# Optimization experiments

Measured on AMD Instinct MI355X. Metric: run time of the kernel, lower is better.

## Reference

```python
import jax, jax.numpy as jnp
import numpy as np

L, B, S, D, F, H = 4, 2, 1024, 1024, 4096, 16
EPS = 1e-5


def setup_inputs() -> dict:
    key = jax.random.key(0)
    ks = jax.random.split(key, 15)
    w = lambda k, shape, s=0.02: (jax.random.normal(k, shape, jnp.float32) * s)
    inp = {
        "x": jax.random.normal(ks[0], (B, S, D), jnp.float32),
        # stacked per-layer params (scanned over leading L axis)
        "ln1_w": jnp.ones((L, D), jnp.float32),
        "ln1_b": jnp.zeros((L, D), jnp.float32),
        "Wq": w(ks[1], (L, D, D)),
        "Wk": w(ks[2], (L, D, D)),
        "Wv": w(ks[3], (L, D, D)),
        "Wo": w(ks[4], (L, D, D)),
        "bo": jnp.zeros((L, D), jnp.float32),
        "ln2_w": jnp.ones((L, D), jnp.float32),
        "ln2_b": jnp.zeros((L, D), jnp.float32),
        "W1": w(ks[5], (L, D, F)),
        "b1": jnp.zeros((L, F), jnp.float32),
        "W2": w(ks[6], (L, F, D)),
        "b2": jnp.zeros((L, D), jnp.float32),
    }
    return inp


def _layernorm(y, w, b):
    m = jnp.mean(y, axis=-1, keepdims=True)
    v = jnp.mean(jnp.square(y - m), axis=-1, keepdims=True)
    return (y - m) * jax.lax.rsqrt(v + EPS) * w + b


def _block(x, p):
    ln1w, ln1b, wq, wk, wv, wo, bo, ln2w, ln2b, w1, b1, w2, b2 = p
    b, s, d = x.shape
    dh = d // H
    scale = dh ** -0.5
    # --- attention sub-block (pre-norm, residual) ---
    h = _layernorm(x, ln1w, ln1b)
    q = (h @ wq).reshape(b, s, H, dh).transpose(0, 2, 1, 3)  # bhsd
    k = (h @ wk).reshape(b, s, H, dh).transpose(0, 2, 1, 3)
    v = (h @ wv).reshape(b, s, H, dh).transpose(0, 2, 1, 3)
    attn = jax.nn.softmax(jnp.einsum("bhqd,bhkd->bhqk", q, k) * scale, axis=-1)
    o = jnp.einsum("bhqk,bhkd->bhqd", attn, v).transpose(0, 2, 1, 3).reshape(b, s, d)
    x = x + (o @ wo + bo)
    # --- FFN sub-block (pre-norm, residual) ---
    h = _layernorm(x, ln2w, ln2b)
    x = x + (jax.nn.gelu(h @ w1 + b1, approximate=False) @ w2 + b2)
    return x, None


def reference(x, ln1_w, ln1_b, Wq, Wk, Wv, Wo, bo, ln2_w, ln2_b, W1, b1, W2, b2):
    xs = (ln1_w, ln1_b, Wq, Wk, Wv, Wo, bo, ln2_w, ln2_b, W1, b1, W2, b2)
    out, _ = jax.lax.scan(_block, x, xs)
    return out
```

## Files before the change

### kernel.cpp

```cpp
#include <hip/hip_runtime.h>
#include <hip/hip_bf16.h>

using bf16   = __bf16;
using bf16x2 = __attribute__((ext_vector_type(2))) __bf16;
using bf16x4 = __attribute__((ext_vector_type(4))) __bf16;
using bf16x8 = __attribute__((ext_vector_type(8))) __bf16;
using f32x4  = __attribute__((ext_vector_type(4))) float;

constexpr int LAYERS = 4;
constexpr int BATCH  = 2;
constexpr int SEQ    = 1024;
constexpr int DIM    = 1024;
constexpr int FF     = 4096;
constexpr int HEADS  = 16;
constexpr int TOK    = BATCH * SEQ;
constexpr int QKVN   = 3 * DIM;
constexpr float EPS  = 1e-5f;

__device__ __forceinline__ void gload_lds16(const void* g, void* l) {
    __builtin_amdgcn_global_load_lds(
        (const __attribute__((address_space(1))) void*)g,
        (__attribute__((address_space(3))) void*)l, 16, 0, 0);
}

__global__ __launch_bounds__(256) void ln_kernel(
    const float* __restrict__ x, const float* __restrict__ g,
    const float* __restrict__ bt, bf16* __restrict__ out)
{
    __shared__ float red[8];
    const int row = blockIdx.x, t = threadIdx.x;
    const float4 v = ((const float4*)(x + (size_t)row * DIM))[t];

    float s = v.x + v.y + v.z + v.w;
    #pragma unroll
    for (int o = 32; o; o >>= 1) s += __shfl_down(s, o, 64);
    if ((t & 63) == 0) red[t >> 6] = s;
    __syncthreads();
    const float mean = (red[0] + red[1] + red[2] + red[3]) * (1.0f / DIM);

    const float dx = v.x - mean, dy = v.y - mean, dz = v.z - mean, dw = v.w - mean;
    float q = dx * dx + dy * dy + dz * dz + dw * dw;
    #pragma unroll
    for (int o = 32; o; o >>= 1) q += __shfl_down(q, o, 64);
    if ((t & 63) == 0) red[4 + (t >> 6)] = q;
    __syncthreads();
    const float var = (red[4] + red[5] + red[6] + red[7]) * (1.0f / DIM);
    const float rstd = rsqrtf(var + EPS);

    const float4 gg = ((const float4*)g)[t];
    const float4 bb = ((const float4*)bt)[t];
    bf16x4 o4;
    o4[0] = (bf16)(dx * rstd * gg.x + bb.x);
    o4[1] = (bf16)(dy * rstd * gg.y + bb.y);
    o4[2] = (bf16)(dz * rstd * gg.z + bb.z);
    o4[3] = (bf16)(dw * rstd * gg.w + bb.w);
    *(bf16x4*)(out + (size_t)row * DIM + t * 4) = o4;
}

template<bool DO_LN>
__global__ __launch_bounds__(256) void lncomb_kernel(
    float* __restrict__ x, const float* __restrict__ p,
    const float* __restrict__ bias, const float* __restrict__ g,
    const float* __restrict__ bt, bf16* __restrict__ out)
{
    __shared__ float red[8];
    const int row = blockIdx.x, t = threadIdx.x;
    float4 v = ((const float4*)(x + (size_t)row * DIM))[t];
    const float4 a0 = ((const float4*)(p + (size_t)row * DIM))[t];
    const float4 a1 = ((const float4*)(p + (size_t)(TOK + row) * DIM))[t];
    const float4 bv = ((const float4*)bias)[t];
    v.x += a0.x + a1.x + bv.x;
    v.y += a0.y + a1.y + bv.y;
    v.z += a0.z + a1.z + bv.z;
    v.w += a0.w + a1.w + bv.w;
    ((float4*)(x + (size_t)row * DIM))[t] = v;
    if (!DO_LN) return;

    float s = v.x + v.y + v.z + v.w;
    #pragma unroll
    for (int o = 32; o; o >>= 1) s += __shfl_down(s, o, 64);
    if ((t & 63) == 0) red[t >> 6] = s;
    __syncthreads();
    const float mean = (red[0] + red[1] + red[2] + red[3]) * (1.0f / DIM);

    const float dx = v.x - mean, dy = v.y - mean, dz = v.z - mean, dw = v.w - mean;
    float q = dx * dx + dy * dy + dz * dz + dw * dw;
    #pragma unroll
    for (int o = 32; o; o >>= 1) q += __shfl_down(q, o, 64);
    if ((t & 63) == 0) red[4 + (t >> 6)] = q;
    __syncthreads();
    const float var = (red[4] + red[5] + red[6] + red[7]) * (1.0f / DIM);
    const float rstd = rsqrtf(var + EPS);

    const float4 gg = ((const float4*)g)[t];
    const float4 bb = ((const float4*)bt)[t];
    bf16x4 o4;
    o4[0] = (bf16)(dx * rstd * gg.x + bb.x);
    o4[1] = (bf16)(dy * rstd * gg.y + bb.y);
    o4[2] = (bf16)(dz * rstd * gg.z + bb.z);
    o4[3] = (bf16)(dw * rstd * gg.w + bb.w);
    *(bf16x4*)(out + (size_t)row * DIM + t * 4) = o4;
}

__global__ __launch_bounds__(256) void wtrans_all_kernel(
    const float* __restrict__ Wq, const float* __restrict__ Wk,
    const float* __restrict__ Wv, const float* __restrict__ Wo,
    const float* __restrict__ W1, const float* __restrict__ W2,
    bf16* __restrict__ wqkvt, bf16* __restrict__ wot,
    bf16* __restrict__ w1t, bf16* __restrict__ w2t)
{
    __shared__ float tile[32][33];
    const int bid = blockIdx.x;
    const float* W; bf16* Wt; int N, K, rowoff, bx, by;
    if (bid < 3072) {
        const int seg = bid >> 10, r = bid & 1023;
        W = (seg == 0) ? Wq : (seg == 1) ? Wk : Wv;
        Wt = wqkvt; N = DIM; K = DIM; rowoff = seg * DIM;
        bx = r & 31; by = r >> 5;
    } else if (bid < 4096) {
        const int r = bid - 3072;
        W = Wo; Wt = wot; N = DIM; K = DIM; rowoff = 0;
        bx = r & 31; by = r >> 5;
    } else if (bid < 8192) {
        const int r = bid - 4096;
        W = W1; Wt = w1t; N = FF; K = DIM; rowoff = 0;
        bx = r & 127; by = r >> 7;
    } else {
        const int r = bid - 8192;
        W = W2; Wt = w2t; N = DIM; K = FF; rowoff = 0;
        bx = r & 31; by = r >> 5;
    }
    const int bn = bx * 32, bk = by * 32;
    const int r = threadIdx.x >> 3, c4 = (threadIdx.x & 7) * 4;
    const float4 v = *(const float4*)(W + (size_t)(bk + r) * N + bn + c4);
    tile[r][c4 + 0] = v.x; tile[r][c4 + 1] = v.y;
    tile[r][c4 + 2] = v.z; tile[r][c4 + 3] = v.w;
    __syncthreads();
    bf16x4 o;
    #pragma unroll
    for (int j = 0; j < 4; ++j) o[j] = (bf16)tile[c4 + j][r];
    *(bf16x4*)(Wt + (size_t)(rowoff + bn + r) * K + bk + c4) = o;
}

template<int BN, int EPI, int SK>
__global__ __launch_bounds__(256) void gemm_kernel(
    const bf16* __restrict__ A, const bf16* __restrict__ Bt,
    const float* __restrict__ bias, void* __restrict__ outv,
    int M, int N, int Kfull)
{
    constexpr int MR  = (BN == 128) ? 4 : 2;
    constexpr int ASZ = 128 * 32, BSZ = BN * 32;
    __shared__ bf16 As[2][ASZ];
    __shared__ bf16 Bs[2][BSZ];

    const int t    = threadIdx.x;
    const int lane = t & 63;
    const int w    = t >> 6;
    const int wm   = (BN == 128) ? (w >> 1) * 64 : w * 32;
    const int wn   = (BN == 128) ? (w & 1) * 64 : 0;
    const int kg   = lane >> 4, lr = lane & 15;

    const int nwg = gridDim.x;
    const int bid = (blockIdx.x & 7) * (nwg >> 3) + (blockIdx.x >> 3);
    const int nbn = N / BN, nbm = M / 128;
    const int ks  = (SK > 1) ? bid / (nbm * nbn) : 0;
    const int r   = (SK > 1) ? bid % (nbm * nbn) : bid;
    const int bm  = ((SK > 1) ? (r / nbn) : (r % nbm)) * 128;
    const int bn  = ((SK > 1) ? (r % nbn) : (r / nbm)) * BN;

    const int Ksl = Kfull / SK;
    const int kof = ks * Ksl;

    f32x4 acc[MR][4] = {};

    auto stage = [&](int buf, int k0) {
        #pragma unroll
        for (int c = 0; c < 2; ++c) {
            const int ci = c * 256 + t;
            gload_lds16(A + (size_t)(bm + (ci >> 2)) * Kfull + kof + k0 + (ci & 3) * 8,
                        &As[buf][ci * 8]);
        }
        #pragma unroll
        for (int c = 0; c < BN / 64; ++c) {
            const int ci = c * 256 + t;
            gload_lds16(Bt + (size_t)(bn + (ci >> 2)) * Kfull + kof + k0 + (ci & 3) * 8,
                        &Bs[buf][ci * 8]);
        }
    };

    stage(0, 0);
    __syncthreads();

    int cur = 0;
    for (int k0 = 0; k0 < Ksl; k0 += 32) {
        if (k0 + 32 < Ksl) stage(cur ^ 1, k0 + 32);

        bf16x8 af[MR], bfr[4];
        #pragma unroll
        for (int m = 0; m < MR; ++m)
            af[m] = *(const bf16x8*)(&As[cur][(wm + m * 16 + lr) * 32 + kg * 8]);
        #pragma unroll
        for (int n = 0; n < 4; ++n)
            bfr[n] = *(const bf16x8*)(&Bs[cur][(wn + n * 16 + lr) * 32 + kg * 8]);
        #pragma unroll
        for (int m = 0; m < MR; ++m)
            #pragma unroll
            for (int n = 0; n < 4; ++n)
                acc[m][n] = __builtin_amdgcn_mfma_f32_16x16x32_bf16(af[m], bfr[n], acc[m][n], 0, 0, 0);

        __syncthreads();
        cur ^= 1;
    }

    #pragma unroll
    for (int m = 0; m < MR; ++m) {
        const int row = bm + wm + m * 16 + kg * 4;
        #pragma unroll
        for (int n = 0; n < 4; ++n) {
            const int col = bn + wn + n * 16 + lr;
            #pragma unroll
            for (int j = 0; j < 4; ++j) {
                const float vv = acc[m][n][j];
                const size_t idx = (size_t)(row + j) * N + col;
                if (EPI == 0) {
                    ((bf16*)outv)[idx] = (bf16)vv;
                } else if (EPI == 1) {
                    const float z = vv + bias[col];
                    const float gl = 0.5f * z * (1.0f + erff(z * 0.70710678118654752f));
                    ((bf16*)outv)[idx] = (bf16)gl;
                } else {
                    ((float*)outv)[(size_t)ks * M * N + idx] = vv;
                }
            }
        }
    }
}

__global__ __launch_bounds__(256) void attn_kernel(
    const bf16* __restrict__ qkv, bf16* __restrict__ od)
{
    __shared__ bf16 Ks[2][64][72];
    __shared__ bf16 Vt[2][64][64];
    __shared__ bf16 Ps[4][16][72];

    const int nwg = gridDim.x;
    const int bid = (blockIdx.x & 7) * (nwg >> 3) + (blockIdx.x >> 3);
    const int q0  = (bid & 15) * 64;
    const int bh  = bid >> 4;
    const int b   = bh >> 4, h = bh & 15;
    const int t   = threadIdx.x, w = t >> 6, lane = t & 63;
    const int kg  = lane >> 4, lr = lane & 15;

    const bf16* qbase = qkv + (size_t)b * SEQ * QKVN + h * 64;
    const bf16* kbase = qbase + DIM;
    const bf16* vbase = qbase + 2 * DIM;

    bf16x8 qf0, qf1;
    {
        const bf16* qr = qbase + (size_t)(q0 + w * 16 + lr) * QKVN;
        qf0 = *(const bf16x8*)(qr + kg * 8);
        qf1 = *(const bf16x8*)(qr + 32 + kg * 8);
        #pragma unroll
        for (int j = 0; j < 8; ++j) {
            qf0[j] = (bf16)((float)qf0[j] * 0.125f);
            qf1[j] = (bf16)((float)qf1[j] * 0.125f);
        }
    }

    f32x4 o_acc[4] = {};
    float m_run = -1e30f, l_run = 0.f;

    const int rK = t >> 3, oK = (t & 7) * 8;
    const int rp = t >> 3, cV = t & 7;

    bf16x8 kr0, kr1, vr0, vr1;
    auto loadKV = [&](int kb) {
        kr0 = *(const bf16x8*)(kbase + (size_t)(kb + rK) * QKVN + oK);
        kr1 = *(const bf16x8*)(kbase + (size_t)(kb + 32 + rK) * QKVN + oK);
        vr0 = *(const bf16x8*)(vbase + (size_t)(kb + 2 * rp) * QKVN + cV * 8);
        vr1 = *(const bf16x8*)(vbase + (size_t)(kb + 2 * rp + 1) * QKVN + cV * 8);
    };
    auto storeKV = [&](int buf) {
        *(bf16x8*)&Ks[buf][rK][oK]      = kr0;
        *(bf16x8*)&Ks[buf][32 + rK][oK] = kr1;
        #pragma unroll
        for (int j = 0; j < 8; ++j) {
            bf16x2 p; p[0] = vr0[j]; p[1] = vr1[j];
            const int d  = cV * 8 + j;
            const int dw = (((rp >> 2) ^ (j ^ cV)) << 2) | (rp & 3);
            *(bf16x2*)((char*)&Vt[buf][d][0] + dw * 4) = p;
        }
    };

    loadKV(0);
    storeKV(0);
    __syncthreads();

    int cur = 0;
    for (int kb = 0; kb < SEQ; kb += 64) {
        const bool more = (kb + 64 < SEQ);
        if (more) loadKV(kb + 64);

        f32x4 s[4] = {};
        #pragma unroll
        for (int n = 0; n < 4; ++n) {
            const bf16x8 kf0 = *(const bf16x8*)&Ks[cur][n * 16 + lr][kg * 8];
            const bf16x8 kf1 = *(const bf16x8*)&Ks[cur][n * 16 + lr][32 + kg * 8];
            s[n] = __builtin_amdgcn_mfma_f32_16x16x32_bf16(kf0, qf0, s[n], 0, 0, 0);
            s[n] = __builtin_amdgcn_mfma_f32_16x16x32_bf16(kf1, qf1, s[n], 0, 0, 0);
        }

        float pmax = -1e30f;
        #pragma unroll
        for (int n = 0; n < 4; ++n)
            #pragma unroll
            for (int j = 0; j < 4; ++j) pmax = fmaxf(pmax, s[n][j]);
        pmax = fmaxf(pmax, __shfl_xor(pmax, 16, 64));
        pmax = fmaxf(pmax, __shfl_xor(pmax, 32, 64));

        if (!__all(pmax <= m_run + 8.0f)) {
            const float mn   = fmaxf(m_run, pmax);
            const float corr = __expf(m_run - mn);
            m_run = mn;
            l_run *= corr;
            #pragma unroll
            for (int nd = 0; nd < 4; ++nd)
                #pragma unroll
                for (int j = 0; j < 4; ++j) o_acc[nd][j] *= corr;
        }

        float rs = 0.f;
        #pragma unroll
        for (int n = 0; n < 4; ++n)
            #pragma unroll
            for (int j = 0; j < 4; ++j) {
                const float e = __expf(s[n][j] - m_run);
                s[n][j] = e; rs += e;
            }
        rs += __shfl_xor(rs, 16, 64);
        rs += __shfl_xor(rs, 32, 64);
        l_run += rs;

        #pragma unroll
        for (int n = 0; n < 4; ++n) {
            bf16x4 pw;
            #pragma unroll
            for (int j = 0; j < 4; ++j) pw[j] = (bf16)s[n][j];
            *(bf16x4*)&Ps[w][lr][n * 16 + kg * 4] = pw;
        }

        const bf16x8 pf0 = *(const bf16x8*)&Ps[w][lr][kg * 8];
        const bf16x8 pf1 = *(const bf16x8*)&Ps[w][lr][32 + kg * 8];
        #pragma unroll
        for (int nd = 0; nd < 4; ++nd) {
            const int d   = nd * 16 + lr;
            const int key = (d ^ (d >> 3)) & 7;
            const bf16x8 vf0 = *(const bf16x8*)((const char*)&Vt[cur][d][0] + ((kg ^ key) << 4));
            const bf16x8 vf1 = *(const bf16x8*)((const char*)&Vt[cur][d][0] + (((4 + kg) ^ key) << 4));
            o_acc[nd] = __builtin_amdgcn_mfma_f32_16x16x32_bf16(vf0, pf0, o_acc[nd], 0, 0, 0);
            o_acc[nd] = __builtin_amdgcn_mfma_f32_16x16x32_bf16(vf1, pf1, o_acc[nd], 0, 0, 0);
        }

        if (more) storeKV(cur ^ 1);
        __syncthreads();
        cur ^= 1;
    }

    const float inv = 1.0f / l_run;
    bf16* ob = od + (size_t)(b * SEQ + q0 + w * 16 + lr) * DIM + h * 64;
    #pragma unroll
    for (int nd = 0; nd < 4; ++nd) {
        bf16x4 o4;
        #pragma unroll
        for (int j = 0; j < 4; ++j) o4[j] = (bf16)(o_acc[nd][j] * inv);
        *(bf16x4*)(ob + nd * 16 + kg * 4) = o4;
    }
}

extern "C" void kernel_launch(void* const* d_in, const int* in_sizes, int n_in,
                              void* d_out, int out_size, void* d_ws, size_t ws_size,
                              hipStream_t stream)
{
    const float* x    = (const float*)d_in[0];
    const float* ln1w = (const float*)d_in[1];
    const float* ln1b = (const float*)d_in[2];
    const float* Wq   = (const float*)d_in[3];
    const float* Wk   = (const float*)d_in[4];
    const float* Wv   = (const float*)d_in[5];
    const float* Wo   = (const float*)d_in[6];
    const float* bo   = (const float*)d_in[7];
    const float* ln2w = (const float*)d_in[8];
    const float* ln2b = (const float*)d_in[9];
    const float* W1   = (const float*)d_in[10];
    const float* b1   = (const float*)d_in[11];
    const float* W2   = (const float*)d_in[12];
    const float* b2   = (const float*)d_in[13];

    char* ws = (char*)d_ws;
    float* xbuf  = (float*)(ws);
    bf16*  hbuf  = (bf16*)(ws + (8ull  << 20));
    bf16*  qkvb  = (bf16*)(ws + (12ull << 20));
    bf16*  obuf  = (bf16*)(ws + (24ull << 20));
    bf16*  gbuf  = (bf16*)(ws + (28ull << 20));
    bf16*  wqkvt = (bf16*)(ws + (44ull << 20));
    bf16*  wot   = (bf16*)(ws + (50ull << 20));
    bf16*  w1t   = (bf16*)(ws + (52ull << 20));
    bf16*  w2t   = (bf16*)(ws + (60ull << 20));
    float* pbuf  = (float*)(ws + (68ull << 20));

    hipMemcpyAsync(xbuf, x, (size_t)TOK * DIM * sizeof(float),
                   hipMemcpyDeviceToDevice, stream);

    const size_t DD = (size_t)DIM * DIM, DF = (size_t)DIM * FF;
    for (int l = 0; l < LAYERS; ++l) {
        wtrans_all_kernel<<<12288, 256, 0, stream>>>(
            Wq + l * DD, Wk + l * DD, Wv + l * DD, Wo + l * DD,
            W1 + l * DF, W2 + l * DF, wqkvt, wot, w1t, w2t);

        if (l == 0)
            ln_kernel<<<TOK, 256, 0, stream>>>(xbuf, ln1w, ln1b, hbuf);

        gemm_kernel<64, 0, 1><<<16 * 48, 256, 0, stream>>>(
            hbuf, wqkvt, nullptr, qkvb, TOK, QKVN, DIM);

        attn_kernel<<<512, 256, 0, stream>>>(qkvb, obuf);

        gemm_kernel<64, 3, 2><<<16 * 8 * 2 * 2, 256, 0, stream>>>(
            obuf, wot, nullptr, pbuf, TOK, DIM, DIM);

        lncomb_kernel<true><<<TOK, 256, 0, stream>>>(
            xbuf, pbuf, bo + l * DIM, ln2w + l * DIM, ln2b + l * DIM, hbuf);

        gemm_kernel<128, 1, 1><<<16 * 32, 256, 0, stream>>>(
            hbuf, w1t, b1 + l * FF, gbuf, TOK, FF, DIM);

        gemm_kernel<64, 3, 2><<<16 * 8 * 2 * 2, 256, 0, stream>>>(
            gbuf, w2t, nullptr, pbuf, TOK, DIM, FF);

        if (l + 1 < LAYERS)
            lncomb_kernel<true><<<TOK, 256, 0, stream>>>(
                xbuf, pbuf, b2 + l * DIM, ln1w + (l + 1) * DIM, ln1b + (l + 1) * DIM, hbuf);
        else
            lncomb_kernel<false><<<TOK, 256, 0, stream>>>(
                xbuf, pbuf, b2 + l * DIM, nullptr, nullptr, nullptr);
    }

    hipMemcpyAsync(d_out, xbuf, (size_t)TOK * DIM * sizeof(float),
                   hipMemcpyDeviceToDevice, stream);
}
```

Before: 650.5 us.

## Deepen GEMM K-tile to 64 with XOR-swizzled LDS and prioritize attention MFMA

The GEMM now stages 64-wide K tiles instead of 32, halving loop iterations and barriers. It applies an XOR swizzle to LDS columns to avoid bank conflicts on fragment reads. The BN=128 variant is dropped, so the FFN1 GEMM runs as 128x64 tiles with twice as many blocks. The attention kernel raises wave priority around its MFMA sections with s_setprio. Doubling LDS per block may reduce occupancy, and the smaller FFN1 tile lowers per-block data reuse.

```diff
diff --git a/kernel.cpp b/kernel.cpp
--- a/kernel.cpp
+++ b/kernel.cpp
@@ -142,31 +142,30 @@
     *(bf16x4*)(Wt + (size_t)(rowoff + bn + r) * K + bk + c4) = o;
 }
 
-template<int BN, int EPI, int SK>
+template<int EPI, int SK>
 __global__ __launch_bounds__(256) void gemm_kernel(
     const bf16* __restrict__ A, const bf16* __restrict__ Bt,
     const float* __restrict__ bias, void* __restrict__ outv,
     int M, int N, int Kfull)
 {
-    constexpr int MR  = (BN == 128) ? 4 : 2;
-    constexpr int ASZ = 128 * 32, BSZ = BN * 32;
-    __shared__ bf16 As[2][ASZ];
-    __shared__ bf16 Bs[2][BSZ];
+    constexpr int MR = 2;
+    __shared__ bf16 As[2][128 * 64];
+    __shared__ bf16 Bs[2][64 * 64];
 
     const int t    = threadIdx.x;
     const int lane = t & 63;
     const int w    = t >> 6;
-    const int wm   = (BN == 128) ? (w >> 1) * 64 : w * 32;
-    const int wn   = (BN == 128) ? (w & 1) * 64 : 0;
+    const int wm   = w * 32;
     const int kg   = lane >> 4, lr = lane & 15;
+    const int key  = lr & 7;
 
     const int nwg = gridDim.x;
     const int bid = (blockIdx.x & 7) * (nwg >> 3) + (blockIdx.x >> 3);
-    const int nbn = N / BN, nbm = M / 128;
+    const int nbn = N / 64, nbm = M / 128;
     const int ks  = (SK > 1) ? bid / (nbm * nbn) : 0;
     const int r   = (SK > 1) ? bid % (nbm * nbn) : bid;
     const int bm  = ((SK > 1) ? (r / nbn) : (r % nbm)) * 128;
-    const int bn  = ((SK > 1) ? (r % nbn) : (r / nbm)) * BN;
+    const int bn  = ((SK > 1) ? (r % nbn) : (r / nbm)) * 64;
 
     const int Ksl = Kfull / SK;
     const int kof = ks * Ksl;
@@ -175,15 +174,15 @@
 
     auto stage = [&](int buf, int k0) {
         #pragma unroll
-        for (int c = 0; c < 2; ++c) {
-            const int ci = c * 256 + t;
-            gload_lds16(A + (size_t)(bm + (ci >> 2)) * Kfull + kof + k0 + (ci & 3) * 8,
+        for (int it = 0; it < 4; ++it) {
+            const int ci = it * 256 + t, row = ci >> 3, c = ci & 7;
+            gload_lds16(A + (size_t)(bm + row) * Kfull + kof + k0 + ((c ^ (row & 7)) << 3),
                         &As[buf][ci * 8]);
         }
         #pragma unroll
-        for (int c = 0; c < BN / 64; ++c) {
-            const int ci = c * 256 + t;
-            gload_lds16(Bt + (size_t)(bn + (ci >> 2)) * Kfull + kof + k0 + (ci & 3) * 8,
+        for (int it = 0; it < 2; ++it) {
+            const int ci = it * 256 + t, row = ci >> 3, c = ci & 7;
+            gload_lds16(Bt + (size_t)(bn + row) * Kfull + kof + k0 + ((c ^ (row & 7)) << 3),
                         &Bs[buf][ci * 8]);
         }
     };
@@ -192,21 +191,28 @@
     __syncthreads();
 
     int cur = 0;
-    for (int k0 = 0; k0 < Ksl; k0 += 32) {
-        if (k0 + 32 < Ksl) stage(cur ^ 1, k0 + 32);
-
-        bf16x8 af[MR], bfr[4];
-        #pragma unroll
-        for (int m = 0; m < MR; ++m)
-            af[m] = *(const bf16x8*)(&As[cur][(wm + m * 16 + lr) * 32 + kg * 8]);
-        #pragma unroll
-        for (int n = 0; n < 4; ++n)
-            bfr[n] = *(const bf16x8*)(&Bs[cur][(wn + n * 16 + lr) * 32 + kg * 8]);
-        #pragma unroll
-        for (int m = 0; m < MR; ++m)
-            #pragma unroll
-            for (int n = 0; n < 4; ++n)
-                acc[m][n] = __builtin_amdgcn_mfma_f32_16x16x32_bf16(af[m], bfr[n], acc[m][n], 0, 0, 0);
+    for (int k0 = 0; k0 < Ksl; k0 += 64) {
+        if (k0 + 64 < Ksl) stage(cur ^ 1, k0 + 64);
+
+        #pragma unroll
+        for (int kk = 0; kk < 2; ++kk) {
+            bf16x8 af[MR], bfr[4];
+            #pragma unroll
+            for (int m = 0; m < MR; ++m) {
+                const int row = wm + m * 16 + lr;
+                af[m] = *(const bf16x8*)(&As[cur][row * 64 + (((kk * 4 + kg) ^ key) << 3)]);
+            }
+            #pragma unroll
+            for (int n = 0; n < 4; ++n) {
+                const int row = n * 16 + lr;
+                bfr[n] = *(const bf16x8*)(&Bs[cur][row * 64 + (((kk * 4 + kg) ^ key) << 3)]);
+            }
+            #pragma unroll
+            for (int m = 0; m < MR; ++m)
+                #pragma unroll
+                for (int n = 0; n < 4; ++n)
+                    acc[m][n] = __builtin_amdgcn_mfma_f32_16x16x32_bf16(af[m], bfr[n], acc[m][n], 0, 0, 0);
+        }
 
         __syncthreads();
         cur ^= 1;
@@ -217,7 +223,7 @@
         const int row = bm + wm + m * 16 + kg * 4;
         #pragma unroll
         for (int n = 0; n < 4; ++n) {
-            const int col = bn + wn + n * 16 + lr;
+            const int col = bn + n * 16 + lr;
             #pragma unroll
             for (int j = 0; j < 4; ++j) {
                 const float vv = acc[m][n][j];
@@ -302,6 +308,7 @@
         if (more) loadKV(kb + 64);
 
         f32x4 s[4] = {};
+        __builtin_amdgcn_s_setprio(1);
         #pragma unroll
         for (int n = 0; n < 4; ++n) {
             const bf16x8 kf0 = *(const bf16x8*)&Ks[cur][n * 16 + lr][kg * 8];
@@ -309,6 +316,7 @@
             s[n] = __builtin_amdgcn_mfma_f32_16x16x32_bf16(kf0, qf0, s[n], 0, 0, 0);
             s[n] = __builtin_amdgcn_mfma_f32_16x16x32_bf16(kf1, qf1, s[n], 0, 0, 0);
         }
+        __builtin_amdgcn_s_setprio(0);
 
         float pmax = -1e30f;
         #pragma unroll
@@ -351,15 +359,17 @@
 
         const bf16x8 pf0 = *(const bf16x8*)&Ps[w][lr][kg * 8];
         const bf16x8 pf1 = *(const bf16x8*)&Ps[w][lr][32 + kg * 8];
+        __builtin_amdgcn_s_setprio(1);
         #pragma unroll
         for (int nd = 0; nd < 4; ++nd) {
             const int d   = nd * 16 + lr;
-            const int key = (d ^ (d >> 3)) & 7;
-            const bf16x8 vf0 = *(const bf16x8*)((const char*)&Vt[cur][d][0] + ((kg ^ key) << 4));
-            const bf16x8 vf1 = *(const bf16x8*)((const char*)&Vt[cur][d][0] + (((4 + kg) ^ key) << 4));
+            const int keyv = (d ^ (d >> 3)) & 7;
+            const bf16x8 vf0 = *(const bf16x8*)((const char*)&Vt[cur][d][0] + ((kg ^ keyv) << 4));
+            const bf16x8 vf1 = *(const bf16x8*)((const char*)&Vt[cur][d][0] + (((4 + kg) ^ keyv) << 4));
             o_acc[nd] = __builtin_amdgcn_mfma_f32_16x16x32_bf16(vf0, pf0, o_acc[nd], 0, 0, 0);
             o_acc[nd] = __builtin_amdgcn_mfma_f32_16x16x32_bf16(vf1, pf1, o_acc[nd], 0, 0, 0);
         }
+        __builtin_amdgcn_s_setprio(0);
 
         if (more) storeKV(cur ^ 1);
         __syncthreads();
@@ -420,21 +430,21 @@
         if (l == 0)
             ln_kernel<<<TOK, 256, 0, stream>>>(xbuf, ln1w, ln1b, hbuf);
 
-        gemm_kernel<64, 0, 1><<<16 * 48, 256, 0, stream>>>(
+        gemm_kernel<0, 1><<<16 * 48, 256, 0, stream>>>(
             hbuf, wqkvt, nullptr, qkvb, TOK, QKVN, DIM);
 
         attn_kernel<<<512, 256, 0, stream>>>(qkvb, obuf);
 
-        gemm_kernel<64, 3, 2><<<16 * 8 * 2 * 2, 256, 0, stream>>>(
+        gemm_kernel<3, 2><<<16 * 16 * 2, 256, 0, stream>>>(
             obuf, wot, nullptr, pbuf, TOK, DIM, DIM);
 
         lncomb_kernel<true><<<TOK, 256, 0, stream>>>(
             xbuf, pbuf, bo + l * DIM, ln2w + l * DIM, ln2b + l * DIM, hbuf);
 
-        gemm_kernel<128, 1, 1><<<16 * 32, 256, 0, stream>>>(
+        gemm_kernel<1, 1><<<16 * 64, 256, 0, stream>>>(
             hbuf, w1t, b1 + l * FF, gbuf, TOK, FF, DIM);
 
-        gemm_kernel<64, 3, 2><<<16 * 8 * 2 * 2, 256, 0, stream>>>(
+        gemm_kernel<3, 2><<<16 * 16 * 2, 256, 0, stream>>>(
             gbuf, w2t, nullptr, pbuf, TOK, DIM, FF);
 
         if (l + 1 < LAYERS)
```

After: 607.1 us. 1.07x faster.
